# Kernel tuning notes

Hardware: AMD Instinct MI355X
Metric: run time of the kernel (lower is better)

Reference implementation:

```python
import jax, jax.numpy as jnp
import numpy as np

NUM_QUERIES = 10000
NUM_CLASSES = 2048
IOU_THRESH = 0.5


def setup_inputs() -> dict:
    key = jax.random.key(0)
    k1, k2, k3, k4 = jax.random.split(key, 4)
    return {
        "pred_logits": jax.random.normal(k1, (1, NUM_QUERIES, NUM_CLASSES), dtype=jnp.float32),
        "pred_boxes": jax.random.uniform(k2, (1, NUM_QUERIES, 4), dtype=jnp.float32),
        "cls_logits": jax.random.normal(k3, (1, NUM_CLASSES), dtype=jnp.float32),
        "target_sizes": jax.random.randint(k4, (1, 2), 480, 1333, dtype=jnp.int64),
    }


def box_cxcywh_to_xyxy(b):
    cx, cy, w, h = b[..., 0], b[..., 1], b[..., 2], b[..., 3]
    return jnp.stack([cx - 0.5 * w, cy - 0.5 * h, cx + 0.5 * w, cy + 0.5 * h], axis=-1)


def nms_keep(boxes, scores, iou_thresh):
    """Greedy NMS; returns a boolean keep mask over the N boxes (xyxy)."""
    n = boxes.shape[0]
    order = jnp.argsort(-scores)
    bs = boxes[order]  # [N,4] sorted by score desc
    areas = jnp.clip(bs[:, 2] - bs[:, 0], 0.0) * jnp.clip(bs[:, 3] - bs[:, 1], 0.0)
    idx = jnp.arange(n)

    def body(i, state):
        keep_s, active = state
        alive = active[i]
        keep_s = keep_s.at[i].set(alive)
        # IoU of box i against all boxes
        lt = jnp.maximum(bs[i, :2], bs[:, :2])
        rb = jnp.minimum(bs[i, 2:], bs[:, 2:])
        wh = jnp.clip(rb - lt, 0.0)
        inter = wh[:, 0] * wh[:, 1]
        iou = inter / (areas[i] + areas - inter)
        suppress = (iou > iou_thresh) & (idx > i) & alive
        return keep_s, active & (~suppress)

    keep_s, _ = jax.lax.fori_loop(
        0, n, body, (jnp.zeros(n, dtype=bool), jnp.ones(n, dtype=bool))
    )
    # map back from sorted order to original order
    return jnp.zeros(n, dtype=bool).at[order].set(keep_s)


def reference(pred_logits, pred_boxes, cls_logits, target_sizes):
    # class scores / labels
    prob = jax.nn.softmax(pred_logits, axis=-1)          # [B,Q,C]
    scores = prob.max(axis=-1)                           # [B,Q]
    labels = prob.argmax(axis=-1)                        # [B,Q]
    cls_preds = jnp.argmax(cls_logits, axis=1)           # [B]

    # boxes: cxcywh -> xyxy, clamp to [0,1], scale to image size
    boxes = jnp.clip(box_cxcywh_to_xyxy(pred_boxes), 0.0, 1.0)  # [B,Q,4]
    ts = target_sizes.astype(jnp.float32)
    img_h, img_w = ts[:, 0], ts[:, 1]
    scale_fct = jnp.stack([img_w, img_h, img_w, img_h], axis=1)  # [B,4]
    boxes = boxes * scale_fct[:, None, :]

    # greedy NMS on batch 0 (module only supports this path for B=1)
    keep = nms_keep(boxes[0], scores.reshape(-1), IOU_THRESH)    # [Q] bool

    return scores[0], labels[0], boxes[0], keep, cls_preds
```

## Files before the change

### kernel.cpp

```cpp
#include <hip/hip_runtime.h>
#include <stdint.h>
#include <math.h>

#define NQ 10000
#define NC 2048
#define NW 157
#define NR 79
#define NTRI 12403
#define IOU_TH 0.5f


__global__ __launch_bounds__(256) void k_front(const float* __restrict__ logits,
        const float* __restrict__ cls, const float* __restrict__ pb,
        const int* __restrict__ ts,
        float* __restrict__ out_scores, float* __restrict__ out_labels,
        float* __restrict__ out_cls, float* __restrict__ out_boxes,
        float* __restrict__ ws_scores, float* __restrict__ boxes4,
        int* __restrict__ rank) {
    int bx = blockIdx.x;
    if (bx < 2500) {
        int wave = threadIdx.x >> 6;
        int lane = threadIdx.x & 63;
        int q = bx * 4 + wave;
        if (q >= NQ) return;
        const float* row = logits + (size_t)q * NC;
        float4 v[8];
        float m = -3.4e38f;
        int am = 0;
        #pragma unroll
        for (int k = 0; k < 8; k++) {
            int idx = k * 256 + lane * 4;
            v[k] = *(const float4*)(row + idx);
            if (v[k].x > m) { m = v[k].x; am = idx; }
            if (v[k].y > m) { m = v[k].y; am = idx + 1; }
            if (v[k].z > m) { m = v[k].z; am = idx + 2; }
            if (v[k].w > m) { m = v[k].w; am = idx + 3; }
        }
        #pragma unroll
        for (int off = 32; off >= 1; off >>= 1) {
            float om = __shfl_xor(m, off);
            int   oa = __shfl_xor(am, off);
            if (om > m || (om == m && oa < am)) { m = om; am = oa; }
        }
        float s = 0.f;
        #pragma unroll
        for (int k = 0; k < 8; k++) {
            s += expf(v[k].x - m);
            s += expf(v[k].y - m);
            s += expf(v[k].z - m);
            s += expf(v[k].w - m);
        }
        #pragma unroll
        for (int off = 32; off >= 1; off >>= 1) s += __shfl_xor(s, off);
        if (lane == 0) {
            float sc = 1.0f / s;
            out_scores[q] = sc;
            out_labels[q] = (float)am;
            ws_scores[q]  = sc;
        }
        return;
    }
    if (bx == 2500) {
        float m = -3.4e38f; int am = 0x7fffffff;
        for (int idx = threadIdx.x; idx < NC; idx += 256) {
            float x = cls[idx];
            if (x > m) { m = x; am = idx; }
        }
        int lane = threadIdx.x & 63, wave = threadIdx.x >> 6;
        #pragma unroll
        for (int off = 32; off >= 1; off >>= 1) {
            float om = __shfl_xor(m, off); int oa = __shfl_xor(am, off);
            if (om > m || (om == m && oa < am)) { m = om; am = oa; }
        }
        __shared__ float sm[4]; __shared__ int sa[4];
        if (lane == 0) { sm[wave] = m; sa[wave] = am; }
        __syncthreads();
        if (threadIdx.x == 0) {
            for (int w = 1; w < 4; w++)
                if (sm[w] > m || (sm[w] == m && sa[w] < am)) { m = sm[w]; am = sa[w]; }
            out_cls[0] = (float)am;
        }
        return;
    }
    {
        #pragma clang fp contract(off)
        int i = (bx - 2501) * 256 + threadIdx.x;
        if (i >= NQ) return;
        rank[i] = 0;
        int a0 = ts[0], a1 = ts[1];
        int ih, iw;
        if (a1 == 0) { ih = a0; iw = ts[2]; } else { ih = a0; iw = a1; }
        float sh = (float)ih, sw = (float)iw;
        float4 b = *(const float4*)(pb + i * 4);
        float x1 = b.x - 0.5f * b.z;
        float y1 = b.y - 0.5f * b.w;
        float x2 = b.x + 0.5f * b.z;
        float y2 = b.y + 0.5f * b.w;
        x1 = fminf(fmaxf(x1, 0.f), 1.f) * sw;
        y1 = fminf(fmaxf(y1, 0.f), 1.f) * sh;
        x2 = fminf(fmaxf(x2, 0.f), 1.f) * sw;
        y2 = fminf(fmaxf(y2, 0.f), 1.f) * sh;
        float4 o = make_float4(x1, y1, x2, y2);
        *(float4*)(out_boxes + i * 4) = o;
        *(float4*)(boxes4 + i * 4) = o;
    }
}

__global__ __launch_bounds__(256) void k_count(const float* __restrict__ scores,
                                               int* __restrict__ rank) {
    __shared__ float4 sc4[500];
    int jbase = blockIdx.y * 2000;
    const float4* src = (const float4*)(scores + jbase);
    for (int t = threadIdx.x; t < 500; t += 256) sc4[t] = src[t];
    __syncthreads();
    int i = blockIdx.x * 256 + threadIdx.x;
    if (i >= NQ) return;
    float si = scores[i];
    int cnt = 0;
    #pragma unroll 2
    for (int q = 0; q < 500; q++) {
        float4 v = sc4[q];
        int j = jbase + 4 * q;
        cnt += (v.x > si) || (v.x == si && j     < i);
        cnt += (v.y > si) || (v.y == si && j + 1 < i);
        cnt += (v.z > si) || (v.z == si && j + 2 < i);
        cnt += (v.w > si) || (v.w == si && j + 3 < i);
    }
    if (cnt) atomicAdd(&rank[i], cnt);
}

__global__ __launch_bounds__(256) void k_scatter(const float* __restrict__ boxes4,
        const int* __restrict__ rank, int* __restrict__ order,
        float* __restrict__ sx1, float* __restrict__ sy1,
        float* __restrict__ sx2, float* __restrict__ sy2,
        float* __restrict__ sarea) {
    #pragma clang fp contract(off)
    int i = blockIdx.x * 256 + threadIdx.x;
    if (i >= NQ) return;
    int r = rank[i];
    order[r] = i;
    float4 b = *(const float4*)(boxes4 + i * 4);
    sx1[r] = b.x; sy1[r] = b.y; sx2[r] = b.z; sy2[r] = b.w;
    sarea[r] = fmaxf(b.z - b.x, 0.f) * fmaxf(b.w - b.y, 0.f);
}

__global__ __launch_bounds__(64) void k_mask(const float* __restrict__ sx1,
        const float* __restrict__ sy1, const float* __restrict__ sx2,
        const float* __restrict__ sy2, const float* __restrict__ sarea,
        unsigned long long* __restrict__ mask) {
    #pragma clang fp contract(off)
    int tri = blockIdx.x;
    int rb = (int)((2.0 * NW + 1.0
              - sqrt((double)((2 * NW + 1) * (2 * NW + 1) - 8 * tri))) * 0.5);
    while (rb > 0 && rb * NW - rb * (rb - 1) / 2 > tri) rb--;
    while ((rb + 1) * NW - (rb + 1) * rb / 2 <= tri) rb++;
    int cb = rb + (tri - (rb * NW - rb * (rb - 1) / 2));

    int t = threadIdx.x;
    __shared__ float cx1[64], cy1[64], cx2[64], cy2[64], ca[64];
    int j0 = cb * 64 + t;
    if (j0 < NQ) { cx1[t]=sx1[j0]; cy1[t]=sy1[j0]; cx2[t]=sx2[j0]; cy2[t]=sy2[j0]; ca[t]=sarea[j0]; }
    __syncthreads();
    int i = rb * 64 + t;
    if (i >= NQ) return;
    float xi1 = sx1[i], yi1 = sy1[i], xi2 = sx2[i], yi2 = sy2[i], ai = sarea[i];
    int ncol = min(64, NQ - cb * 64);
    unsigned long long word = 0;
    for (int jj = 0; jj < ncol; jj++) {
        int j = cb * 64 + jj;
        float lx = fmaxf(xi1, cx1[jj]);
        float ly = fmaxf(yi1, cy1[jj]);
        float rx = fminf(xi2, cx2[jj]);
        float ry = fminf(yi2, cy2[jj]);
        float w = fmaxf(rx - lx, 0.f);
        float h = fmaxf(ry - ly, 0.f);
        float inter = w * h;
        float denom = (ai + ca[jj]) - inter;
        float iou = inter / denom;
        bool sup = (iou > IOU_TH) && (j > i);
        word |= ((unsigned long long)(sup ? 1u : 0u)) << jj;
    }
    mask[(size_t)i * NW + cb] = word;
}

__device__ __forceinline__ unsigned long long bcast64(unsigned long long v) {
    uint32_t lo = (uint32_t)__builtin_amdgcn_readfirstlane((int)(uint32_t)v);
    uint32_t hi = (uint32_t)__builtin_amdgcn_readfirstlane((int)(uint32_t)(v >> 32));
    return ((unsigned long long)hi << 32) | lo;
}

__global__ __launch_bounds__(256, 1) void k_scan(const unsigned long long* __restrict__ mask,
        const int* __restrict__ order, float* __restrict__ out_keep) {
    __shared__ unsigned long long rem[NW];
    __shared__ unsigned long long keepw[NW];
    __shared__ unsigned long long stA[2][4][64];
    __shared__ unsigned long long stB[2][3][64];
    __shared__ unsigned long long sh_k0, sh_k1;

    const int tid  = threadIdx.x;
    const int wave = tid >> 6;
    const int lane = tid & 63;

    for (int w = tid; w < NW; w += 256) rem[w] = 0;

    uint64_t sA0=0,sA1=0,sA2=0,sA3=0,sB0=0,sB1=0,sB2=0;

    if (wave == 1) {
        {
            const unsigned long long* rp = mask + (size_t)lane * NW;
            stA[0][0][lane]=rp[0]; stA[0][1][lane]=rp[1];
            stA[0][2][lane]=rp[2]; stA[0][3][lane]=rp[3];
            const unsigned long long* rq = mask + (size_t)(64 + lane) * NW;
            stB[0][0][lane]=rq[1]; stB[0][1][lane]=rq[2]; stB[0][2][lane]=rq[3];
        }
        {
            const unsigned long long* rp = mask + (size_t)(128 + lane) * NW + 2;
            sA0=rp[0]; sA1=rp[1]; sA2=rp[2]; sA3=rp[3];
            const unsigned long long* rq = mask + (size_t)(192 + lane) * NW + 3;
            sB0=rq[0]; sB1=rq[1]; sB2=rq[2];
        }
    }
    __syncthreads();

    uint64_t pp0=0,pp1=0,pp2=0,pp3=0,pp4=0,pp5=0,pp6=0,pp7=0;
    uint64_t pp8=0,pp9=0,pp10=0,pp11=0,pp12=0,pp13=0,pp14=0,pp15=0;
    uint64_t pp16=0,pp17=0,pp18=0,pp19=0,pp20=0,pp21=0,pp22=0,pp23=0;
    uint64_t pp24=0,pp25=0,pp26=0,pp27=0,pp28=0,pp29=0,pp30=0,pp31=0;
    uint64_t pex = 0;
    int pw = -1;

    uint64_t kept0 = 0, kept1 = 0;

    for (int r = 0; r < NR; r++) {
        const int a = 2 * r, b = a + 1;
        const int par = r & 1;

        if (wave == 0) {
            uint64_t remA_v = rem[a];
            uint64_t remB_v = (b < NW) ? rem[b] : ~0ull;
            uint64_t dgA = stA[par][0][lane];
            uint64_t xAB = stA[par][1][lane];
            uint64_t dgB = (b < NW) ? stB[par][0][lane] : 0;
            uint64_t dfA = dgA | (1ull << lane);
            uint64_t dfB = dgB | (1ull << lane);

            uint64_t cur0 = bcast64(remA_v);
            int nv0 = min(64, NQ - a * 64);
            if (nv0 < 64) cur0 |= (~0ull) << nv0;
            uint32_t dflo = (uint32_t)dfA, dfhi = (uint32_t)(dfA >> 32);
            uint32_t xlo  = (uint32_t)xAB, xhi  = (uint32_t)(xAB >> 32);
            uint64_t alive = ~cur0;
            uint64_t k0 = 0, AcB = 0;
            while (alive) {
                int bb = (int)__builtin_ctzll(alive);
                uint64_t df = ((uint64_t)(uint32_t)__builtin_amdgcn_readlane((int)dfhi, bb) << 32)
                            | (uint32_t)__builtin_amdgcn_readlane((int)dflo, bb);
                uint64_t x  = ((uint64_t)(uint32_t)__builtin_amdgcn_readlane((int)xhi, bb) << 32)
                            | (uint32_t)__builtin_amdgcn_readlane((int)xlo, bb);
                k0    |= 1ull << bb;
                cur0  |= df;
                AcB   |= x;
                alive &= ~df;
            }
            cur0 &= ~k0;
            kept0 = k0;

            uint64_t k1 = 0, cur1 = 0;
            if (b < NW) {
                cur1 = bcast64(remB_v) | AcB;
                int nv1 = min(64, NQ - b * 64);
                if (nv1 < 64) cur1 |= (~0ull) << nv1;
                uint32_t blo = (uint32_t)dfB, bhi = (uint32_t)(dfB >> 32);
                uint64_t alv = ~cur1;
                while (alv) {
                    int bb = (int)__builtin_ctzll(alv);
                    uint64_t df = ((uint64_t)(uint32_t)__builtin_amdgcn_readlane((int)bhi, bb) << 32)
                                | (uint32_t)__builtin_amdgcn_readlane((int)blo, bb);
                    k1  |= 1ull << bb;
                    cur1 |= df;
                    alv &= ~df;
                }
                cur1 &= ~k1;
            }
            kept1 = k1;
            if (tid == 0) {
                sh_k0 = k0; sh_k1 = k1;
                keepw[a] = cur0;
                if (b < NW) keepw[b] = cur1;
            }
        } else {
            if (pw >= 0) {
                uint64_t pacc = (((pp0|pp1)|(pp2|pp3)) | ((pp4|pp5)|(pp6|pp7)))
                              | (((pp8|pp9)|(pp10|pp11)) | ((pp12|pp13)|(pp14|pp15)));
                pacc |= (((pp16|pp17)|(pp18|pp19)) | ((pp20|pp21)|(pp22|pp23)))
                      | (((pp24|pp25)|(pp26|pp27)) | ((pp28|pp29)|(pp30|pp31)));
                pacc |= pex;
                if (pacc) atomicOr(&rem[pw], (unsigned long long)pacc);
            }
            pw = -1;
        }
        __syncthreads();

        const int c2 = a + 2, c3 = a + 3;
        if (wave == 0) {
            if (c2 < NW) {
                uint64_t vA2 = stA[par][2][lane];
                uint64_t vB1 = (b < NW) ? stB[par][1][lane] : 0;
                uint64_t m2 = (((kept0 >> lane) & 1ull) ? vA2 : 0)
                            | (((kept1 >> lane) & 1ull) ? vB1 : 0);
                uint64_t m3 = 0;
                if (c3 < NW) {
                    uint64_t vA3 = stA[par][3][lane];
                    uint64_t vB2 = (b < NW) ? stB[par][2][lane] : 0;
                    m3 = (((kept0 >> lane) & 1ull) ? vA3 : 0)
                       | (((kept1 >> lane) & 1ull) ? vB2 : 0);
                }
                #pragma unroll
                for (int off = 32; off >= 1; off >>= 1) {
                    m2 |= __shfl_xor(m2, off);
                    m3 |= __shfl_xor(m3, off);
                }
                if (lane == 0) {
                    rem[c2] |= m2;
                    if (c3 < NW) rem[c3] |= m3;
                }
            }
        } else {
            uint64_t k0 = bcast64(sh_k0);
            uint64_t k1 = bcast64(sh_k1);

            if (wave == 1) {
                int par2 = (r + 1) & 1;
                stA[par2][0][lane]=sA0; stA[par2][1][lane]=sA1;
                stA[par2][2][lane]=sA2; stA[par2][3][lane]=sA3;
                stB[par2][0][lane]=sB0; stB[par2][1][lane]=sB1; stB[par2][2][lane]=sB2;
                sA0=sA1=sA2=sA3=sB0=sB1=sB2=0;
                int rr = r + 2;
                if (rr < NR) {
                    int a2 = 2 * rr, b2 = a2 + 1;
                    int ra = a2 * 64 + lane, rbw = b2 * 64 + lane;
                    if (a2 < NW && ra < NQ) {
                        const unsigned long long* rp = mask + (size_t)ra * NW + a2;
                        sA0 = rp[0];
                        if (a2 + 1 < NW) sA1 = rp[1];
                        if (a2 + 2 < NW) sA2 = rp[2];
                        if (a2 + 3 < NW) sA3 = rp[3];
                    }
                    if (b2 < NW && rbw < NQ) {
                        const unsigned long long* rq = mask + (size_t)rbw * NW + b2;
                        sB0 = rq[0];
                        if (b2 + 1 < NW) sB1 = rq[1];
                        if (b2 + 2 < NW) sB2 = rq[2];
                    }
                }
            }

            int w = a + 4 + (tid - 64);
            if ((k0 | k1) && w < NW) {
                const unsigned long long* baseA = mask + (size_t)(a * 64) * NW + w;
                const unsigned long long* baseB = mask + (size_t)(b * 64) * NW + w;
                uint64_t km0 = k0, km1 = k1;
                const unsigned long long* fb =
                    km0 ? baseA + (size_t)__builtin_ctzll(km0) * NW
                        : baseB + (size_t)__builtin_ctzll(km1) * NW;
                #define BULK_SLOT(P) { const unsigned long long* rp; \
                    if (km0)      { rp = baseA + (size_t)__builtin_ctzll(km0) * NW; km0 &= km0 - 1; } \
                    else if (km1) { rp = baseB + (size_t)__builtin_ctzll(km1) * NW; km1 &= km1 - 1; } \
                    else rp = fb; \
                    P = rp[0]; }
                BULK_SLOT(pp0)  BULK_SLOT(pp1)  BULK_SLOT(pp2)  BULK_SLOT(pp3)
                BULK_SLOT(pp4)  BULK_SLOT(pp5)  BULK_SLOT(pp6)  BULK_SLOT(pp7)
                BULK_SLOT(pp8)  BULK_SLOT(pp9)  BULK_SLOT(pp10) BULK_SLOT(pp11)
                BULK_SLOT(pp12) BULK_SLOT(pp13) BULK_SLOT(pp14) BULK_SLOT(pp15)
                BULK_SLOT(pp16) BULK_SLOT(pp17) BULK_SLOT(pp18) BULK_SLOT(pp19)
                BULK_SLOT(pp20) BULK_SLOT(pp21) BULK_SLOT(pp22) BULK_SLOT(pp23)
                BULK_SLOT(pp24) BULK_SLOT(pp25) BULK_SLOT(pp26) BULK_SLOT(pp27)
                BULK_SLOT(pp28) BULK_SLOT(pp29) BULK_SLOT(pp30) BULK_SLOT(pp31)
                pex = 0;
                while (km0 | km1) {
                    uint64_t x0,x1,x2,x3,x4,x5,x6,x7;
                    BULK_SLOT(x0) BULK_SLOT(x1) BULK_SLOT(x2) BULK_SLOT(x3)
                    BULK_SLOT(x4) BULK_SLOT(x5) BULK_SLOT(x6) BULK_SLOT(x7)
                    pex |= (x0|x1)|(x2|x3)|((x4|x5)|(x6|x7));
                }
                #undef BULK_SLOT
                pw = w;
            } else {
                pw = -1; pex = 0;
            }
        }
        __syncthreads();
    }

    for (int si = tid; si < NQ; si += 256) {
        unsigned long long kw = keepw[si >> 6];
        out_keep[order[si]] = ((kw >> (si & 63)) & 1ull) ? 0.f : 1.f;
    }
}

extern "C" void kernel_launch(void* const* d_in, const int* in_sizes, int n_in,
                              void* d_out, int out_size, void* d_ws, size_t ws_size,
                              hipStream_t stream) {
    const float* pred_logits = (const float*)d_in[0];
    const float* pred_boxes  = (const float*)d_in[1];
    const float* cls_logits  = (const float*)d_in[2];
    const int*   tsizes      = (const int*)d_in[3];

    float* out = (float*)d_out;
    float* out_scores = out;
    float* out_labels = out + 10000;
    float* out_boxes  = out + 20000;
    float* out_keep   = out + 60000;
    float* out_cls    = out + 70000;

    char* ws = (char*)d_ws;
    float* ws_scores = (float*)(ws + 0);
    int*   rank      = (int*)  (ws + 40000);
    float* boxes4    = (float*)(ws + 80000);
    float* sx1       = (float*)(ws + 240000);
    float* sy1       = (float*)(ws + 280000);
    float* sx2       = (float*)(ws + 320000);
    float* sy2       = (float*)(ws + 360000);
    float* sarea     = (float*)(ws + 400000);
    int*   order     = (int*)  (ws + 440000);
    unsigned long long* mask = (unsigned long long*)(ws + 480000);

    k_front<<<2541, 256, 0, stream>>>(pred_logits, cls_logits, pred_boxes, tsizes,
                                      out_scores, out_labels, out_cls, out_boxes,
                                      ws_scores, boxes4, rank);
    k_count<<<dim3(40, 5), 256, 0, stream>>>(ws_scores, rank);
    k_scatter<<<40, 256, 0, stream>>>(boxes4, rank, order, sx1, sy1, sx2, sy2, sarea);
    k_mask<<<NTRI, 64, 0, stream>>>(sx1, sy1, sx2, sy2, sarea, mask);
    k_scan<<<1, 256, 0, stream>>>(mask, order, out_keep);
}
```

Before: 423.8 us.

## Restructure NMS scan loop to one barrier per round with register-carried near-word masks

Reworks the serial NMS bitmask scan so each two-word round ends with a single barrier instead of two. Wave 0 keeps the suppression bits for the next two words in registers instead of writing them to shared memory. Wave 1 loads the next staging tile directly within the round instead of software-pipelining it through registers. The bulk OR over far words is now done and applied atomically in the same round, split across threads by kept-set when few words remain, with a smaller unroll. The aim is to shorten the serial critical path per round. The risk is that cross-round races on rem and the double-buffered keep masks are now covered only by the one remaining barrier.

```diff
diff --git a/kernel.cpp b/kernel.cpp
--- a/kernel.cpp
+++ b/kernel.cpp
@@ -195,7 +195,7 @@
     __shared__ unsigned long long keepw[NW];
     __shared__ unsigned long long stA[2][4][64];
     __shared__ unsigned long long stB[2][3][64];
-    __shared__ unsigned long long sh_k0, sh_k1;
+    __shared__ unsigned long long sh_k0p[2], sh_k1p[2];
 
     const int tid  = threadIdx.x;
     const int wave = tid >> 6;
@@ -203,33 +203,18 @@
 
     for (int w = tid; w < NW; w += 256) rem[w] = 0;
 
-    uint64_t sA0=0,sA1=0,sA2=0,sA3=0,sB0=0,sB1=0,sB2=0;
-
     if (wave == 1) {
-        {
-            const unsigned long long* rp = mask + (size_t)lane * NW;
-            stA[0][0][lane]=rp[0]; stA[0][1][lane]=rp[1];
-            stA[0][2][lane]=rp[2]; stA[0][3][lane]=rp[3];
-            const unsigned long long* rq = mask + (size_t)(64 + lane) * NW;
-            stB[0][0][lane]=rq[1]; stB[0][1][lane]=rq[2]; stB[0][2][lane]=rq[3];
-        }
-        {
-            const unsigned long long* rp = mask + (size_t)(128 + lane) * NW + 2;
-            sA0=rp[0]; sA1=rp[1]; sA2=rp[2]; sA3=rp[3];
-            const unsigned long long* rq = mask + (size_t)(192 + lane) * NW + 3;
-            sB0=rq[0]; sB1=rq[1]; sB2=rq[2];
-        }
+        const unsigned long long* rp = mask + (size_t)lane * NW;
+        stA[0][0][lane]=rp[0]; stA[0][1][lane]=rp[1];
+        stA[0][2][lane]=rp[2]; stA[0][3][lane]=rp[3];
+        const unsigned long long* rq = mask + (size_t)(64 + lane) * NW;
+        stB[0][0][lane]=rq[1]; stB[0][1][lane]=rq[2]; stB[0][2][lane]=rq[3];
     }
     __syncthreads();
 
-    uint64_t pp0=0,pp1=0,pp2=0,pp3=0,pp4=0,pp5=0,pp6=0,pp7=0;
-    uint64_t pp8=0,pp9=0,pp10=0,pp11=0,pp12=0,pp13=0,pp14=0,pp15=0;
-    uint64_t pp16=0,pp17=0,pp18=0,pp19=0,pp20=0,pp21=0,pp22=0,pp23=0;
-    uint64_t pp24=0,pp25=0,pp26=0,pp27=0,pp28=0,pp29=0,pp30=0,pp31=0;
-    uint64_t pex = 0;
-    int pw = -1;
-
     uint64_t kept0 = 0, kept1 = 0;
+    uint64_t m2c = 0, m3c = 0;
+    uint64_t vA2 = 0, vA3 = 0, vB1 = 0, vB2 = 0;
 
     for (int r = 0; r < NR; r++) {
         const int a = 2 * r, b = a + 1;
@@ -240,11 +225,18 @@
             uint64_t remB_v = (b < NW) ? rem[b] : ~0ull;
             uint64_t dgA = stA[par][0][lane];
             uint64_t xAB = stA[par][1][lane];
-            uint64_t dgB = (b < NW) ? stB[par][0][lane] : 0;
+            vA2 = stA[par][2][lane];
+            vA3 = stA[par][3][lane];
+            uint64_t dgB = 0;
+            if (b < NW) {
+                dgB = stB[par][0][lane];
+                vB1 = stB[par][1][lane];
+                vB2 = stB[par][2][lane];
+            } else { vB1 = 0; vB2 = 0; }
             uint64_t dfA = dgA | (1ull << lane);
             uint64_t dfB = dgB | (1ull << lane);
 
-            uint64_t cur0 = bcast64(remA_v);
+            uint64_t cur0 = bcast64(remA_v | m2c);
             int nv0 = min(64, NQ - a * 64);
             if (nv0 < 64) cur0 |= (~0ull) << nv0;
             uint32_t dflo = (uint32_t)dfA, dfhi = (uint32_t)(dfA >> 32);
@@ -267,7 +259,7 @@
 
             uint64_t k1 = 0, cur1 = 0;
             if (b < NW) {
-                cur1 = bcast64(remB_v) | AcB;
+                cur1 = bcast64(remB_v | m3c) | AcB;
                 int nv1 = min(64, NQ - b * 64);
                 if (nv1 < 64) cur1 |= (~0ull) << nv1;
                 uint32_t blo = (uint32_t)dfB, bhi = (uint32_t)(dfB >> 32);
@@ -284,114 +276,89 @@
             }
             kept1 = k1;
             if (tid == 0) {
-                sh_k0 = k0; sh_k1 = k1;
+                sh_k0p[par] = k0; sh_k1p[par] = k1;
                 keepw[a] = cur0;
                 if (b < NW) keepw[b] = cur1;
             }
+        } else if (wave == 1) {
+            int a2 = a + 2, b2 = a + 3;
+            if (a2 < NW) {
+                uint64_t A0=0,A1=0,A2v=0,A3v=0,B0=0,B1=0,B2v=0;
+                int ra = a2 * 64 + lane;
+                if (ra < NQ) {
+                    const unsigned long long* rp = mask + (size_t)ra * NW + a2;
+                    A0 = rp[0];
+                    if (a2 + 1 < NW) A1  = rp[1];
+                    if (a2 + 2 < NW) A2v = rp[2];
+                    if (a2 + 3 < NW) A3v = rp[3];
+                }
+                int rb2 = b2 * 64 + lane;
+                if (b2 < NW && rb2 < NQ) {
+                    const unsigned long long* rq = mask + (size_t)rb2 * NW + b2;
+                    B0 = rq[0];
+                    if (b2 + 1 < NW) B1  = rq[1];
+                    if (b2 + 2 < NW) B2v = rq[2];
+                }
+                int p2 = par ^ 1;
+                stA[p2][0][lane]=A0; stA[p2][1][lane]=A1;
+                stA[p2][2][lane]=A2v; stA[p2][3][lane]=A3v;
+                stB[p2][0][lane]=B0; stB[p2][1][lane]=B1; stB[p2][2][lane]=B2v;
+            }
+        }
+        __syncthreads();
+
+        if (wave == 0) {
+            uint64_t m2 = (((kept0 >> lane) & 1ull) ? vA2 : 0)
+                        | (((kept1 >> lane) & 1ull) ? vB1 : 0);
+            uint64_t m3 = (((kept0 >> lane) & 1ull) ? vA3 : 0)
+                        | (((kept1 >> lane) & 1ull) ? vB2 : 0);
+            #pragma unroll
+            for (int off = 32; off >= 1; off >>= 1) {
+                m2 |= __shfl_xor(m2, off);
+                m3 |= __shfl_xor(m3, off);
+            }
+            m2c = m2; m3c = m3;
         } else {
-            if (pw >= 0) {
-                uint64_t pacc = (((pp0|pp1)|(pp2|pp3)) | ((pp4|pp5)|(pp6|pp7)))
-                              | (((pp8|pp9)|(pp10|pp11)) | ((pp12|pp13)|(pp14|pp15)));
-                pacc |= (((pp16|pp17)|(pp18|pp19)) | ((pp20|pp21)|(pp22|pp23)))
-                      | (((pp24|pp25)|(pp26|pp27)) | ((pp28|pp29)|(pp30|pp31)));
-                pacc |= pex;
-                if (pacc) atomicOr(&rem[pw], (unsigned long long)pacc);
-            }
-            pw = -1;
-        }
-        __syncthreads();
-
-        const int c2 = a + 2, c3 = a + 3;
-        if (wave == 0) {
-            if (c2 < NW) {
-                uint64_t vA2 = stA[par][2][lane];
-                uint64_t vB1 = (b < NW) ? stB[par][1][lane] : 0;
-                uint64_t m2 = (((kept0 >> lane) & 1ull) ? vA2 : 0)
-                            | (((kept1 >> lane) & 1ull) ? vB1 : 0);
-                uint64_t m3 = 0;
-                if (c3 < NW) {
-                    uint64_t vA3 = stA[par][3][lane];
-                    uint64_t vB2 = (b < NW) ? stB[par][2][lane] : 0;
-                    m3 = (((kept0 >> lane) & 1ull) ? vA3 : 0)
-                       | (((kept1 >> lane) & 1ull) ? vB2 : 0);
+            uint64_t k0 = bcast64(sh_k0p[par]);
+            uint64_t k1 = bcast64(sh_k1p[par]);
+            int ti = tid - 64;
+            int w0w = a + 4;
+            int nwr = NW - w0w;
+            if ((k0 | k1) && nwr > 0) {
+                int w; uint64_t km0, km1;
+                if (nwr <= 96) {
+                    if (ti < 96) { w = w0w + ti;       km0 = k0; km1 = 0; }
+                    else         { w = w0w + (ti-96);  km0 = 0;  km1 = k1; }
+                } else {
+                    w = w0w + ti; km0 = k0; km1 = k1;
                 }
-                #pragma unroll
-                for (int off = 32; off >= 1; off >>= 1) {
-                    m2 |= __shfl_xor(m2, off);
-                    m3 |= __shfl_xor(m3, off);
+                if (w < NW && (km0 | km1)) {
+                    const unsigned long long* baseA = mask + (size_t)(a * 64) * NW + w;
+                    const unsigned long long* baseB = mask + (size_t)(b * 64) * NW + w;
+                    uint64_t acc = 0;
+                    while (km0 | km1) {
+                        const unsigned long long* fb =
+                            km0 ? baseA + (size_t)__builtin_ctzll(km0) * NW
+                                : baseB + (size_t)__builtin_ctzll(km1) * NW;
+                        uint64_t x0,x1,x2,x3,x4,x5,x6,x7,x8,x9,x10,x11,x12,x13,x14,x15;
+                        #define GS(P) { const unsigned long long* rp; \
+                            if (km0)      { rp = baseA + (size_t)__builtin_ctzll(km0) * NW; km0 &= km0 - 1; } \
+                            else if (km1) { rp = baseB + (size_t)__builtin_ctzll(km1) * NW; km1 &= km1 - 1; } \
+                            else rp = fb; \
+                            P = rp[0]; }
+                        GS(x0)  GS(x1)  GS(x2)  GS(x3)  GS(x4)  GS(x5)  GS(x6)  GS(x7)
+                        GS(x8)  GS(x9)  GS(x10) GS(x11) GS(x12) GS(x13) GS(x14) GS(x15)
+                        #undef GS
+                        acc |= ((x0|x1)|(x2|x3)) | ((x4|x5)|(x6|x7));
+                        acc |= ((x8|x9)|(x10|x11)) | ((x12|x13)|(x14|x15));
+                    }
+                    if (acc) atomicOr(&rem[w], (unsigned long long)acc);
                 }
-                if (lane == 0) {
-                    rem[c2] |= m2;
-                    if (c3 < NW) rem[c3] |= m3;
-                }
-            }
-        } else {
-            uint64_t k0 = bcast64(sh_k0);
-            uint64_t k1 = bcast64(sh_k1);
-
-            if (wave == 1) {
-                int par2 = (r + 1) & 1;
-                stA[par2][0][lane]=sA0; stA[par2][1][lane]=sA1;
-                stA[par2][2][lane]=sA2; stA[par2][3][lane]=sA3;
-                stB[par2][0][lane]=sB0; stB[par2][1][lane]=sB1; stB[par2][2][lane]=sB2;
-                sA0=sA1=sA2=sA3=sB0=sB1=sB2=0;
-                int rr = r + 2;
-                if (rr < NR) {
-                    int a2 = 2 * rr, b2 = a2 + 1;
-                    int ra = a2 * 64 + lane, rbw = b2 * 64 + lane;
-                    if (a2 < NW && ra < NQ) {
-                        const unsigned long long* rp = mask + (size_t)ra * NW + a2;
-                        sA0 = rp[0];
-                        if (a2 + 1 < NW) sA1 = rp[1];
-                        if (a2 + 2 < NW) sA2 = rp[2];
-                        if (a2 + 3 < NW) sA3 = rp[3];
-                    }
-                    if (b2 < NW && rbw < NQ) {
-                        const unsigned long long* rq = mask + (size_t)rbw * NW + b2;
-                        sB0 = rq[0];
-                        if (b2 + 1 < NW) sB1 = rq[1];
-                        if (b2 + 2 < NW) sB2 = rq[2];
-                    }
-                }
-            }
-
-            int w = a + 4 + (tid - 64);
-            if ((k0 | k1) && w < NW) {
-                const unsigned long long* baseA = mask + (size_t)(a * 64) * NW + w;
-                const unsigned long long* baseB = mask + (size_t)(b * 64) * NW + w;
-                uint64_t km0 = k0, km1 = k1;
-                const unsigned long long* fb =
-                    km0 ? baseA + (size_t)__builtin_ctzll(km0) * NW
-                        : baseB + (size_t)__builtin_ctzll(km1) * NW;
-                #define BULK_SLOT(P) { const unsigned long long* rp; \
-                    if (km0)      { rp = baseA + (size_t)__builtin_ctzll(km0) * NW; km0 &= km0 - 1; } \
-                    else if (km1) { rp = baseB + (size_t)__builtin_ctzll(km1) * NW; km1 &= km1 - 1; } \
-                    else rp = fb; \
-                    P = rp[0]; }
-                BULK_SLOT(pp0)  BULK_SLOT(pp1)  BULK_SLOT(pp2)  BULK_SLOT(pp3)
-                BULK_SLOT(pp4)  BULK_SLOT(pp5)  BULK_SLOT(pp6)  BULK_SLOT(pp7)
-                BULK_SLOT(pp8)  BULK_SLOT(pp9)  BULK_SLOT(pp10) BULK_SLOT(pp11)
-                BULK_SLOT(pp12) BULK_SLOT(pp13) BULK_SLOT(pp14) BULK_SLOT(pp15)
-                BULK_SLOT(pp16) BULK_SLOT(pp17) BULK_SLOT(pp18) BULK_SLOT(pp19)
-                BULK_SLOT(pp20) BULK_SLOT(pp21) BULK_SLOT(pp22) BULK_SLOT(pp23)
-                BULK_SLOT(pp24) BULK_SLOT(pp25) BULK_SLOT(pp26) BULK_SLOT(pp27)
-                BULK_SLOT(pp28) BULK_SLOT(pp29) BULK_SLOT(pp30) BULK_SLOT(pp31)
-                pex = 0;
-                while (km0 | km1) {
-                    uint64_t x0,x1,x2,x3,x4,x5,x6,x7;
-                    BULK_SLOT(x0) BULK_SLOT(x1) BULK_SLOT(x2) BULK_SLOT(x3)
-                    BULK_SLOT(x4) BULK_SLOT(x5) BULK_SLOT(x6) BULK_SLOT(x7)
-                    pex |= (x0|x1)|(x2|x3)|((x4|x5)|(x6|x7));
-                }
-                #undef BULK_SLOT
-                pw = w;
-            } else {
-                pw = -1; pex = 0;
-            }
-        }
-        __syncthreads();
-    }
-
+            }
+        }
+    }
+
+    __syncthreads();
     for (int si = tid; si < NQ; si += 256) {
         unsigned long long kw = keepw[si >> 6];
         out_keep[order[si]] = ((kw >> (si & 63)) & 1ull) ? 0.f : 1.f;
```

Measured after the change: 442.0 us. 1.04x slower.
